# Kernel optimization log

Hardware: AMD Instinct MI355X
Metric: run time of the kernel (lower is better)

Reference implementation:

```python
import jax, jax.numpy as jnp
import numpy as np
from jax import lax


def _layernorm(x, scale, bias, eps=1e-5):
    m = x.mean(-1, keepdims=True)
    v = x.var(-1, keepdims=True)
    return (x - m) / jnp.sqrt(v + eps) * scale + bias


def setup_inputs() -> dict:
    key = jax.random.key(0)
    d = 21                      # code distance
    S = d * d - 1               # 440 tokens
    g = d + 1                   # 22x22 grid
    D, H, F, L, B = 256, 8, 512, 6, 64
    ks = jax.random.split(key, 24)
    w = 0.02
    idx = np.arange(S)
    scatter_positions = jnp.asarray(np.stack([idx // g, idx % g], axis=1), dtype=jnp.int64)
    inp = {
        'x': jax.random.randint(ks[0], (B, S), 0, 2).astype(jnp.int64),
        'scatter_positions': scatter_positions,
        'event_emb': w * jax.random.normal(ks[1], (2, D), jnp.float32),
        'pos_x': w * jax.random.normal(ks[2], (2 * d + 1, D), jnp.float32),
        'pos_y': w * jax.random.normal(ks[3], (2 * d + 1, D), jnp.float32),
        'stab_emb': w * jax.random.normal(ks[4], (2, D), jnp.float32),
        'tok_x': jax.random.randint(ks[5], (S,), 0, 2 * d + 1).astype(jnp.int64),
        'tok_y': jax.random.randint(ks[6], (S,), 0, 2 * d + 1).astype(jnp.int64),
        'tok_stab': jax.random.randint(ks[7], (S,), 0, 2).astype(jnp.int64),
        'attn_bias': w * jax.random.normal(ks[8], (S, S), jnp.float32),
        'Wqkv': w * jax.random.normal(ks[9], (L, 3 * D, D), jnp.float32),
        'bqkv': jnp.zeros((L, 3 * D), jnp.float32),
        'Wo': w * jax.random.normal(ks[10], (L, D, D), jnp.float32),
        'bo': jnp.zeros((L, D), jnp.float32),
        'W1': w * jax.random.normal(ks[11], (L, F, D), jnp.float32),
        'b1': jnp.zeros((L, F), jnp.float32),
        'W2': w * jax.random.normal(ks[12], (L, D, F), jnp.float32),
        'b2': jnp.zeros((L, D), jnp.float32),
        'ln1_s': jnp.ones((L, D), jnp.float32),
        'ln1_b': jnp.zeros((L, D), jnp.float32),
        'ln2_s': jnp.ones((L, D), jnp.float32),
        'ln2_b': jnp.zeros((L, D), jnp.float32),
        'cw1': w * jax.random.normal(ks[13], (L, D, D // H, 3, 3), jnp.float32),
        'cb1': jnp.zeros((L, D), jnp.float32),
        'cw2': w * jax.random.normal(ks[14], (L, D, D // H, 3, 3), jnp.float32),
        'cb2': jnp.zeros((L, D), jnp.float32),
        'cw3': w * jax.random.normal(ks[15], (L, D, D // H, 3, 3), jnp.float32),
        'cb3': jnp.zeros((L, D), jnp.float32),
    }
    return inp


def _forward(x, scatter_positions, event_emb, pos_x, pos_y, stab_emb, tok_x, tok_y,
             tok_stab, attn_bias, Wqkv, bqkv, Wo, bo, W1, b1, W2, b2,
             ln1_s, ln1_b, ln2_s, ln2_b, cw1, cb1, cw2, cb2, cw3, cb3):
    B, S = x.shape
    D = event_emb.shape[1]
    L = Wqkv.shape[0]
    H = D // cw1.shape[2]           # groups = n_heads
    dh = D // H
    g = int(np.sqrt(S + 1)) + 1     # (d+1) grid side
    rows = scatter_positions[:, 0]
    cols = scatter_positions[:, 1]

    # 2D positional encoding gathers + event embedding
    pos = pos_x[tok_x] + pos_y[tok_y] + stab_emb[tok_stab]   # [S, D]
    h = event_emb[x] + pos[None]                             # [B, S, D]

    scale = 1.0 / np.sqrt(dh).astype(np.float32)

    def conv(xg, wgt, b, dil):
        y = lax.conv_general_dilated(
            xg, wgt, window_strides=(1, 1), padding=[(dil, dil), (dil, dil)],
            rhs_dilation=(dil, dil), feature_group_count=H,
            dimension_numbers=('NCHW', 'OIHW', 'NCHW'))
        return jax.nn.relu(y + b[None, :, None, None])

    for l in range(L):
        # --- bias-MHA: QK^T * scale + learned relative bias, softmax, V ---
        qkv = jnp.einsum('bsd,ed->bse', h, Wqkv[l]) + bqkv[l]
        q, k, v = jnp.split(qkv, 3, axis=-1)
        q = q.reshape(B, S, H, dh)
        k = k.reshape(B, S, H, dh)
        v = v.reshape(B, S, H, dh)
        scores = jnp.einsum('bqhd,bkhd->bhqk', q, k) * scale + attn_bias[None, None]
        p = jax.nn.softmax(scores, axis=-1)
        o = jnp.einsum('bhqk,bkhd->bqhd', p, v).reshape(B, S, D)
        a = jnp.einsum('bsd,ed->bse', o, Wo[l]) + bo[l]
        h = _layernorm(h + a, ln1_s[l], ln1_b[l])
        # --- FFN (post-norm, ReLU) ---
        ff = jax.nn.relu(jnp.einsum('bsd,fd->bsf', h, W1[l]) + b1[l])
        ff = jnp.einsum('bsf,df->bsd', ff, W2[l]) + b2[l]
        h = _layernorm(h + ff, ln2_s[l], ln2_b[l])
        # --- scatter to 2D grid, grouped dilated convs, collect back ---
        grid = jnp.zeros((B, g, g, D), h.dtype).at[:, rows, cols].set(h)
        xg = grid.transpose(0, 3, 1, 2)                       # NCHW
        xg = 0.5 * (xg + conv(xg, cw1[l], cb1[l], 1)
                       + conv(xg, cw2[l], cb2[l], 2)
                       + conv(xg, cw3[l], cb3[l], 3))
        h = xg.transpose(0, 2, 3, 1)[:, rows, cols]           # collect_from_2d
    return h


def reference(x, scatter_positions, event_emb, pos_x, pos_y, stab_emb, tok_x, tok_y,
              tok_stab, attn_bias, Wqkv, bqkv, Wo, bo, W1, b1, W2, b2,
              ln1_s, ln1_b, ln2_s, ln2_b, cw1, cb1, cw2, cb2, cw3, cb3):
    return _forward(x, scatter_positions, event_emb, pos_x, pos_y, stab_emb, tok_x,
                    tok_y, tok_stab, attn_bias, Wqkv, bqkv, Wo, bo, W1, b1, W2, b2,
                    ln1_s, ln1_b, ln2_s, ln2_b, cw1, cb1, cw2, cb2, cw3, cb3)
```

## Files before the change

### kernel.cpp

```cpp
#include <hip/hip_runtime.h>
#include <hip/hip_bf16.h>

#define NB 64
#define S 440
#define D 256
#define H 8
#define DH 32
#define F 512
#define NL 6
#define G 22
#define NT (NB*S)
#define QBLK 224
#define QT2 2
#define PADK 456
#define CSTR 40

typedef __hip_bfloat16 bf16;
typedef unsigned short u16;
typedef __bf16 bf16x8 __attribute__((ext_vector_type(8)));
typedef float f32x4 __attribute__((ext_vector_type(4)));

#define MAGIC_BF16 0x3F803F80u

__device__ __align__(16) u16 g_abT[(S / 4) * S * 4];
#define WOFF_QKV 0
#define WOFF_WO  (NL*3*D*D)
#define WOFF_W1  (WOFF_WO + NL*D*D)
#define WOFF_W2  (WOFF_W1 + NL*F*D)
__device__ __align__(16) u16 g_wlin[WOFF_W2 + NL*D*F];
#define CVSTRIDE ((size_t)NL * 9 * 8 * 1024)
__device__ __align__(16) u16 g_cwt[3 * CVSTRIDE];
__device__ __align__(16) u16 g_qkvb[(size_t)NT * 768];
__device__ __align__(16) u16 g_obuf[(size_t)NT * D];
__device__ __align__(16) u16 g_acb [(size_t)NT * D];
__device__ __align__(16) u16 g_hbb [(size_t)NT * D];

static __device__ __forceinline__ float bf2f(bf16 x) { return __bfloat162float(x); }
static __device__ __forceinline__ float u2f(u16 u) {
  union { unsigned int i; float f; } t; t.i = ((unsigned int)u) << 16; return t.f;
}
static __device__ __forceinline__ float i2f(unsigned v) {
  union { unsigned u; float f; } t; t.u = v; return t.f;
}
static __device__ __forceinline__ u16 f2u(float f) {
  bf16 h = __float2bfloat16(f);
  return *(u16*)&h;
}
static __device__ __forceinline__ unsigned cvt_pk(float lo, float hi) {
  unsigned r;
  asm("v_cvt_pk_bf16_f32 %0, %1, %2" : "=v"(r) : "v"(lo), "v"(hi));
  return r;
}
static __device__ __forceinline__ float ldT(const void* p, size_t i, bool bfm) {
  return bfm ? u2f(((const u16*)p)[i]) : ((const float*)p)[i];
}
static __device__ __forceinline__ bf16x8 as_bf16x8(uint4 v) {
  union { uint4 u; bf16x8 b; } t; t.u = v; return t.b;
}
static __device__ __forceinline__ void gload_lds16(const u16* g, u16* l) {
  __builtin_amdgcn_global_load_lds(
      (const __attribute__((address_space(1))) void*)g,
      (__attribute__((address_space(3))) void*)l, 16, 0, 0);
}
static __device__ __forceinline__ const u16* selbuf(const void* ext, int sel) {
  return sel == 0 ? (const u16*)ext : sel == 1 ? g_hbb : sel == 2 ? g_qkvb : g_obuf;
}

__global__ void __launch_bounds__(256) cvt_conv(
    const void* __restrict__ src, int which, const unsigned* __restrict__ probe)
{
  bool bfm = (*probe == MAGIC_BF16);
  int n = NL * D * DH * 9;
  int i = blockIdx.x * 256 + threadIdx.x;
  if (i >= n) return;
  int kk = i % 9;
  int ic = (i / 9) % DH;
  int oc = (i / 288) % D;
  int l  = i / 73728;
  int g = oc >> 5, oc32 = oc & 31;
  u16 v;
  if (bfm) v = ((const u16*)src)[i];
  else     v = f2u(((const float*)src)[i]);
  g_cwt[(size_t)which * CVSTRIDE + (((size_t)l * 9 + kk) * 8 + g) * 1024 + oc32 * 32 + ic] = v;
}

__global__ void __launch_bounds__(256) cvt_lin(
    const void* __restrict__ src, size_t dstoff, int n,
    const unsigned* __restrict__ probe)
{
  bool bfm = (*probe == MAGIC_BF16);
  int i = blockIdx.x * 256 + threadIdx.x;
  if (i >= n) return;
  g_wlin[dstoff + i] = bfm ? ((const u16*)src)[i] : f2u(((const float*)src)[i]);
}

__global__ void __launch_bounds__(256) cvt_bias(
    const void* __restrict__ ab, const unsigned* __restrict__ probe)
{
  bool bfm = (*probe == MAGIC_BF16);
  int i = blockIdx.x * 256 + threadIdx.x;
  if (i >= (S / 4) * S * 4) return;
  int j = i & 3;
  int t = i >> 2;
  int q = t % S;
  int k4 = t / S;
  int k = k4 * 4 + j;
  float v = ldT(ab, (size_t)q * S + k, bfm) * 1.4426950408889634f;
  g_abT[i] = f2u(v);
}

__global__ void __launch_bounds__(256) embed_kernel(
    const int* __restrict__ x, const void* __restrict__ event_emb,
    const void* __restrict__ pos_x, const void* __restrict__ pos_y,
    const void* __restrict__ stab_emb, const int* __restrict__ tok_x,
    const int* __restrict__ tok_y, const int* __restrict__ tok_stab,
    bf16* __restrict__ h, const unsigned* __restrict__ probe)
{
  bool bfm = (*probe == MAGIC_BF16);
  int d = threadIdx.x;
#pragma unroll
  for (int r = 0; r < 4; ++r) {
    int t = blockIdx.x * 4 + r;
    int b = t / S, s = t - b * S;
    float v = ldT(event_emb, (size_t)x[b * S + s] * D + d, bfm)
            + ldT(pos_x, (size_t)tok_x[s] * D + d, bfm)
            + ldT(pos_y, (size_t)tok_y[s] * D + d, bfm)
            + ldT(stab_emb, (size_t)tok_stab[s] * D + d, bfm);
    h[(size_t)t * D + d] = __float2bfloat16(v);
  }
}

template <int RELU>
__global__ void __launch_bounds__(256) gemm_mfma(
    const void* __restrict__ Aext, int asel, size_t woff,
    const void* __restrict__ bias, size_t boff, int csel,
    int M, int N, int K, const unsigned* __restrict__ probe)
{
  bool bfm = (*probe == MAGIC_BF16);
  __shared__ u16 As[2][128][32];
  __shared__ u16 Ws[2][128][32];
  int tid = threadIdx.x;
  int bn = blockIdx.x, bm = blockIdx.y;
  int lane = tid & 63, w = tid >> 6;
  int wm = (w >> 1) * 64, wn = (w & 1) * 64;
  int qd = lane >> 4, ln16 = lane & 15;
  f32x4 zero4 = {0.f, 0.f, 0.f, 0.f};
  f32x4 acc[4][4];
#pragma unroll
  for (int i = 0; i < 4; ++i)
#pragma unroll
    for (int j = 0; j < 4; ++j) acc[i][j] = zero4;

  const u16* Au = selbuf(Aext, asel);
  u16* Cu = (csel == 0) ? g_qkvb : g_acb;
  const u16* Wu = g_wlin + woff;
  int srow = w * 32 + (lane >> 2);
  int skc  = (lane & 3) << 3;
  size_t abase = (size_t)(bm * 128 + srow) * K + skc;
  size_t wbase = (size_t)(bn * 128 + srow) * K + skc;

  gload_lds16(Au + abase,                   &As[0][w * 32][0]);
  gload_lds16(Au + abase + (size_t)16 * K,  &As[0][w * 32 + 16][0]);
  gload_lds16(Wu + wbase,                   &Ws[0][w * 32][0]);
  gload_lds16(Wu + wbase + (size_t)16 * K,  &Ws[0][w * 32 + 16][0]);

  int cur = 0;
  for (int k0 = 0; k0 < K; k0 += 32) {
    __syncthreads();
    if (k0 + 32 < K) {
      int nb = cur ^ 1;
      gload_lds16(Au + abase + k0 + 32,                  &As[nb][w * 32][0]);
      gload_lds16(Au + abase + (size_t)16 * K + k0 + 32, &As[nb][w * 32 + 16][0]);
      gload_lds16(Wu + wbase + k0 + 32,                  &Ws[nb][w * 32][0]);
      gload_lds16(Wu + wbase + (size_t)16 * K + k0 + 32, &Ws[nb][w * 32 + 16][0]);
    }
    bf16x8 af[4], bfr[4];
#pragma unroll
    for (int t = 0; t < 4; ++t) {
      af[t]  = *(const bf16x8*)&As[cur][wm + t * 16 + ln16][qd * 8];
      bfr[t] = *(const bf16x8*)&Ws[cur][wn + t * 16 + ln16][qd * 8];
    }
#pragma unroll
    for (int mt = 0; mt < 4; ++mt)
#pragma unroll
      for (int nt = 0; nt < 4; ++nt)
        acc[mt][nt] = __builtin_amdgcn_mfma_f32_16x16x32_bf16(af[mt], bfr[nt], acc[mt][nt], 0, 0, 0);
    cur ^= 1;
  }
#pragma unroll
  for (int nt = 0; nt < 4; ++nt) {
    int gcol = bn * 128 + wn + nt * 16 + ln16;
    float bv = ldT(bias, boff + gcol, bfm);
#pragma unroll
    for (int mt = 0; mt < 4; ++mt) {
#pragma unroll
      for (int r = 0; r < 4; ++r) {
        int grow = bm * 128 + wm + mt * 16 + qd * 4 + r;
        float v = acc[mt][nt][r] + bv;
        if (RELU) v = fmaxf(v, 0.f);
        Cu[(size_t)grow * N + gcol] = f2u(v);
      }
    }
  }
}

__global__ void __launch_bounds__(512) gemm_ln(
    const void* __restrict__ Aext, int asel, size_t woff,
    const void* __restrict__ bias, size_t boff,
    void* __restrict__ hext, int hsel,
    const void* __restrict__ sc, size_t soff,
    const void* __restrict__ bi, size_t boff2,
    int K, const unsigned* __restrict__ probe)
{
  bool bfm = (*probe == MAGIC_BF16);
  __shared__ u16 As[2][128][32];
  __shared__ u16 Ws[2][256][32];
  __shared__ float redS[4][128];
  __shared__ float redQ[4][128];
  int tid = threadIdx.x;
  int bm = blockIdx.x;
  int lane = tid & 63, w = tid >> 6;
  int wm = (w >> 2) * 64, wn = (w & 3) * 64;
  int qd = lane >> 4, ln16 = lane & 15;
  f32x4 zero4 = {0.f, 0.f, 0.f, 0.f};
  f32x4 acc[4][4];
#pragma unroll
  for (int i = 0; i < 4; ++i)
#pragma unroll
    for (int j = 0; j < 4; ++j) acc[i][j] = zero4;

  const u16* Au = selbuf(Aext, asel);
  u16* hp = hsel ? g_hbb : (u16*)hext;
  const u16* Wu = g_wlin + woff;
  int arow = w * 16 + (lane >> 2);
  int wrow = w * 32 + (lane >> 2);
  int skc  = (lane & 3) << 3;
  size_t abase = (size_t)(bm * 128 + arow) * K + skc;
  size_t wbase = (size_t)wrow * K + skc;

  gload_lds16(Au + abase,                  &As[0][w * 16][0]);
  gload_lds16(Wu + wbase,                  &Ws[0][w * 32][0]);
  gload_lds16(Wu + wbase + (size_t)16 * K, &Ws[0][w * 32 + 16][0]);

  int cur = 0;
  for (int k0 = 0; k0 < K; k0 += 32) {
    __syncthreads();
    if (k0 + 32 < K) {
      int nb = cur ^ 1;
      gload_lds16(Au + abase + k0 + 32,                  &As[nb][w * 16][0]);
      gload_lds16(Wu + wbase + k0 + 32,                  &Ws[nb][w * 32][0]);
      gload_lds16(Wu + wbase + (size_t)16 * K + k0 + 32, &Ws[nb][w * 32 + 16][0]);
    }
    bf16x8 af[4], bfr[4];
#pragma unroll
    for (int t = 0; t < 4; ++t) {
      af[t]  = *(const bf16x8*)&As[cur][wm + t * 16 + ln16][qd * 8];
      bfr[t] = *(const bf16x8*)&Ws[cur][wn + t * 16 + ln16][qd * 8];
    }
#pragma unroll
    for (int mt = 0; mt < 4; ++mt)
#pragma unroll
      for (int nt = 0; nt < 4; ++nt)
        acc[mt][nt] = __builtin_amdgcn_mfma_f32_16x16x32_bf16(af[mt], bfr[nt], acc[mt][nt], 0, 0, 0);
    cur ^= 1;
  }

  float bv[4];
#pragma unroll
  for (int nt = 0; nt < 4; ++nt) bv[nt] = ldT(bias, boff + wn + nt * 16 + ln16, bfm);
#pragma unroll
  for (int mt = 0; mt < 4; ++mt)
#pragma unroll
    for (int r = 0; r < 4; ++r) {
      size_t grow = (size_t)bm * 128 + wm + mt * 16 + qd * 4 + r;
#pragma unroll
      for (int nt = 0; nt < 4; ++nt) {
        int col = wn + nt * 16 + ln16;
        acc[mt][nt][r] += bv[nt] + u2f(hp[grow * D + col]);
      }
    }
#pragma unroll
  for (int mt = 0; mt < 4; ++mt)
#pragma unroll
    for (int r = 0; r < 4; ++r) {
      float s = (acc[mt][0][r] + acc[mt][1][r]) + (acc[mt][2][r] + acc[mt][3][r]);
      float q = (acc[mt][0][r] * acc[mt][0][r] + acc[mt][1][r] * acc[mt][1][r])
              + (acc[mt][2][r] * acc[mt][2][r] + acc[mt][3][r] * acc[mt][3][r]);
#pragma unroll
      for (int m = 1; m <= 8; m <<= 1) {
        s += __shfl_xor(s, m, 64);
        q += __shfl_xor(q, m, 64);
      }
      if (ln16 == 0) {
        int lrow = wm + mt * 16 + qd * 4 + r;
        redS[w & 3][lrow] = s;
        redQ[w & 3][lrow] = q;
      }
    }
  __syncthreads();
  float ls[4], lb[4];
#pragma unroll
  for (int nt = 0; nt < 4; ++nt) {
    ls[nt] = ldT(sc, soff + wn + nt * 16 + ln16, bfm);
    lb[nt] = ldT(bi, boff2 + wn + nt * 16 + ln16, bfm);
  }
#pragma unroll
  for (int mt = 0; mt < 4; ++mt)
#pragma unroll
    for (int r = 0; r < 4; ++r) {
      int lrow = wm + mt * 16 + qd * 4 + r;
      float Ssum = (redS[0][lrow] + redS[1][lrow]) + (redS[2][lrow] + redS[3][lrow]);
      float Qsum = (redQ[0][lrow] + redQ[1][lrow]) + (redQ[2][lrow] + redQ[3][lrow]);
      float mean = Ssum * (1.0f / D);
      float rstd = rsqrtf(Qsum * (1.0f / D) - mean * mean + 1e-5f);
      size_t grow = (size_t)bm * 128 + lrow;
#pragma unroll
      for (int nt = 0; nt < 4; ++nt) {
        int col = wn + nt * 16 + ln16;
        float o = (acc[mt][nt][r] - mean) * rstd * ls[nt] + lb[nt];
        hp[grow * D + col] = f2u(o);
      }
    }
}

__global__ void __launch_bounds__(448) attn_mfma()
{
  __shared__ u16 VT[32 * PADK];
  int tid = threadIdx.x;
  int blk = blockIdx.x;
  int qt = (blk >> 3) & 1;
  int bh = ((blk >> 4) << 3) | (blk & 7);
  int hh = bh % H;
  int b  = bh / H;
  int lane = tid & 63, w = tid >> 6;
  int qd = lane >> 4, ln16 = lane & 15;
  const u16* qkvu = g_qkvb;

  unsigned* VT32 = (unsigned*)VT;
#pragma unroll
  for (int i = 0; i < 2; ++i) {
    int slot = tid + i * 448;
    int rp = slot >> 2, kc = slot & 3;
    int r0 = rp * 2;
    uint4 va = make_uint4(0, 0, 0, 0), vb = make_uint4(0, 0, 0, 0);
    if (r0 < S)     va = *(const uint4*)&qkvu[((size_t)(b * S + r0)) * 768 + 512 + hh * DH + kc * 8];
    if (r0 + 1 < S) vb = *(const uint4*)&qkvu[((size_t)(b * S + r0 + 1)) * 768 + 512 + hh * DH + kc * 8];
    unsigned aw[4] = {va.x, va.y, va.z, va.w};
    unsigned bw[4] = {vb.x, vb.y, vb.z, vb.w};
#pragma unroll
    for (int jj = 0; jj < 4; ++jj) {
      int d = kc * 8 + jj * 2;
      VT32[(size_t)(d    ) * (PADK / 2) + rp] = (aw[jj] & 0xffffu) | ((bw[jj] & 0xffffu) << 16);
      VT32[(size_t)(d + 1) * (PADK / 2) + rp] = (aw[jj] >> 16)     | ((bw[jj] >> 16) << 16);
    }
  }

  int q0 = qt * QBLK + w * 32;
  int qaA = q0 + ln16;      if (qaA >= S) qaA = S - 1;
  int qaB = q0 + 16 + ln16; if (qaB >= S) qaB = S - 1;
  bf16x8 afA = *(const bf16x8*)&qkvu[((size_t)(b * S + qaA)) * 768 + hh * DH + qd * 8];
  bf16x8 afB = *(const bf16x8*)&qkvu[((size_t)(b * S + qaB)) * 768 + hh * DH + qd * 8];
  __syncthreads();

  int kperm = ((ln16 >> 2) << 3) + (ln16 & 3);
  auto kload = [&](int ks_, int half) -> uint4 {
    int tok = ks_ * 32 + kperm + half * 4;
    if (tok >= S) tok = S - 1;
    return *(const uint4*)&qkvu[((size_t)(b * S + tok)) * 768 + 256 + hh * DH + qd * 8];
  };
  uint4 kn0 = kload(0, 0), kn1 = kload(0, 1);

  float lsA = 0.f, lsB = 0.f;
  f32x4 zero4 = {0.f, 0.f, 0.f, 0.f};
  f32x4 oa0A = zero4, oa1A = zero4;
  f32x4 oa0B = zero4, oa1B = zero4;
  const float SC2 = 0.17677669529663689f * 1.4426950408889634f;

  auto bias4 = [&](uint2 wv, float* o) {
    o[0] = i2f(wv.x << 16); o[1] = i2f(wv.x & 0xffff0000u);
    o[2] = i2f(wv.y << 16); o[3] = i2f(wv.y & 0xffff0000u);
  };

  auto body = [&](int ks, bool masked) {
    int k4a = ks * 8 + 2 * qd;
    int k4b = k4a + 1;
    if (masked) { if (k4a > 109) k4a = 109; if (k4b > 109) k4b = 109; }
    uint2 bwaA = *(const uint2*)&g_abT[((size_t)k4a * S + qaA) * 4];
    uint2 bwbA = *(const uint2*)&g_abT[((size_t)k4b * S + qaA) * 4];
    uint2 bwaB = *(const uint2*)&g_abT[((size_t)k4a * S + qaB) * 4];
    uint2 bwbB = *(const uint2*)&g_abT[((size_t)k4b * S + qaB) * 4];
    bf16x8 kf0 = as_bf16x8(kn0), kf1 = as_bf16x8(kn1);
    if (!masked) { kn0 = kload(ks + 1, 0); kn1 = kload(ks + 1, 1); }
    __builtin_amdgcn_s_setprio(1);
    f32x4 s0A = __builtin_amdgcn_mfma_f32_16x16x32_bf16(kf0, afA, zero4, 0, 0, 0);
    f32x4 s1A = __builtin_amdgcn_mfma_f32_16x16x32_bf16(kf1, afA, zero4, 0, 0, 0);
    f32x4 s0B = __builtin_amdgcn_mfma_f32_16x16x32_bf16(kf0, afB, zero4, 0, 0, 0);
    f32x4 s1B = __builtin_amdgcn_mfma_f32_16x16x32_bf16(kf1, afB, zero4, 0, 0, 0);
    __builtin_amdgcn_s_setprio(0);
    float bAA[4], bBA[4], bAB[4], bBB[4];
    bias4(bwaA, bAA); bias4(bwbA, bBA); bias4(bwaB, bAB); bias4(bwbB, bBB);
    float pA[8], pB[8];
    if (!masked) {
#pragma unroll
      for (int r = 0; r < 4; ++r) {
        pA[r]     = exp2f(fminf(fmaf(s0A[r], SC2, bAA[r]), 80.f));
        pA[4 + r] = exp2f(fminf(fmaf(s1A[r], SC2, bBA[r]), 80.f));
        pB[r]     = exp2f(fminf(fmaf(s0B[r], SC2, bAB[r]), 80.f));
        pB[4 + r] = exp2f(fminf(fmaf(s1B[r], SC2, bBB[r]), 80.f));
      }
    } else {
      int c0 = ks * 32 + qd * 8;
#pragma unroll
      for (int r = 0; r < 4; ++r) {
        bool m0 = (c0 + r < S), m1 = (c0 + 4 + r < S);
        pA[r]     = exp2f(m0 ? fminf(fmaf(s0A[r], SC2, bAA[r]), 80.f) : -1e30f);
        pA[4 + r] = exp2f(m1 ? fminf(fmaf(s1A[r], SC2, bBA[r]), 80.f) : -1e30f);
        pB[r]     = exp2f(m0 ? fminf(fmaf(s0B[r], SC2, bAB[r]), 80.f) : -1e30f);
        pB[4 + r] = exp2f(m1 ? fminf(fmaf(s1B[r], SC2, bBB[r]), 80.f) : -1e30f);
      }
    }
    lsA += ((pA[0] + pA[1]) + (pA[2] + pA[3])) + ((pA[4] + pA[5]) + (pA[6] + pA[7]));
    lsB += ((pB[0] + pB[1]) + (pB[2] + pB[3])) + ((pB[4] + pB[5]) + (pB[6] + pB[7]));
    bf16x8 pfA = as_bf16x8(make_uint4(
        cvt_pk(pA[0], pA[1]), cvt_pk(pA[2], pA[3]),
        cvt_pk(pA[4], pA[5]), cvt_pk(pA[6], pA[7])));
    bf16x8 pfB = as_bf16x8(make_uint4(
        cvt_pk(pB[0], pB[1]), cvt_pk(pB[2], pB[3]),
        cvt_pk(pB[4], pB[5]), cvt_pk(pB[6], pB[7])));
    int kb = ks * 32;
    bf16x8 vf0 = *(const bf16x8*)&VT[(size_t)ln16 * PADK + kb + qd * 8];
    bf16x8 vf1 = *(const bf16x8*)&VT[(size_t)(16 + ln16) * PADK + kb + qd * 8];
    __builtin_amdgcn_s_setprio(1);
    oa0A = __builtin_amdgcn_mfma_f32_16x16x32_bf16(vf0, pfA, oa0A, 0, 0, 0);
    oa1A = __builtin_amdgcn_mfma_f32_16x16x32_bf16(vf1, pfA, oa1A, 0, 0, 0);
    oa0B = __builtin_amdgcn_mfma_f32_16x16x32_bf16(vf0, pfB, oa0B, 0, 0, 0);
    oa1B = __builtin_amdgcn_mfma_f32_16x16x32_bf16(vf1, pfB, oa1B, 0, 0, 0);
    __builtin_amdgcn_s_setprio(0);
  };

  for (int ks = 0; ks < 13; ++ks) body(ks, false);
  body(13, true);

  lsA += __shfl_xor(lsA, 16, 64);
  lsA += __shfl_xor(lsA, 32, 64);
  lsB += __shfl_xor(lsB, 16, 64);
  lsB += __shfl_xor(lsB, 32, 64);
  float invA = 1.0f / lsA, invB = 1.0f / lsB;
  int qA = q0 + ln16, qB = q0 + 16 + ln16;
  if (qA < S) {
    u16* op = g_obuf + ((size_t)(b * S + qA)) * D + hh * DH;
    *(uint2*)&op[qd * 4] = make_uint2(
        cvt_pk(oa0A[0] * invA, oa0A[1] * invA),
        cvt_pk(oa0A[2] * invA, oa0A[3] * invA));
    *(uint2*)&op[16 + qd * 4] = make_uint2(
        cvt_pk(oa1A[0] * invA, oa1A[1] * invA),
        cvt_pk(oa1A[2] * invA, oa1A[3] * invA));
  }
  if (qB < S) {
    u16* op = g_obuf + ((size_t)(b * S + qB)) * D + hh * DH;
    *(uint2*)&op[qd * 4] = make_uint2(
        cvt_pk(oa0B[0] * invB, oa0B[1] * invB),
        cvt_pk(oa0B[2] * invB, oa0B[3] * invB));
    *(uint2*)&op[16 + qd * 4] = make_uint2(
        cvt_pk(oa1B[0] * invB, oa1B[1] * invB),
        cvt_pk(oa1B[2] * invB, oa1B[3] * invB));
  }
}

__global__ void __launch_bounds__(256) conv_mfma(
    const void* __restrict__ hin_ext, int hinsel,
    const void* __restrict__ cb1, const void* __restrict__ cb2,
    const void* __restrict__ cb3, size_t cboff,
    void* __restrict__ hout_ext, int houtsel, int l, int final_,
    const unsigned* __restrict__ probe)
{
  bool bfm = (*probe == MAGIC_BF16);
  __shared__ u16 X[17 * 28 * CSTR];
  int half = blockIdx.x, g = blockIdx.y, b = blockIdx.z;
  int tid = threadIdx.x;
  int rb = half ? 7 : -3;
  const u16* hin = selbuf(hin_ext, hinsel);

  for (int i = tid; i < 17 * 28 * CSTR / 8; i += 256)
    *(uint4*)&X[i * 8] = make_uint4(0, 0, 0, 0);
  __syncthreads();
  int rv0 = half ? 7 : 0;
  int nrow = half ? 13 : 14;
  for (int i = tid; i < nrow * 22 * 4; i += 256) {
    int tk = i >> 2, ch = i & 3;
    int r = rv0 + tk / 22, c = tk % 22;
    uint4 v = *(const uint4*)&hin[((size_t)(b * S + r * 22 + c)) * D + g * 32 + ch * 8];
    *(uint4*)&X[(((r - rb) * 28) + (c + 3)) * CSTR + ch * 8] = v;
  }
  __syncthreads();

  int lane = tid & 63, w = tid >> 6;
  int qd = lane >> 4, ln16 = lane & 15;
  int nt = w & 1;
  int mq = w >> 1;
  int t_base = half * 224 + mq * 112;
  int oc_l = nt * 16 + ln16;

  int aoff[7];
#pragma unroll
  for (int mt = 0; mt < 7; ++mt) {
    int t = t_base + mt * 16 + ln16;
    if (t > S - 1) t = S - 1;
    int r = t / 22, c = t - r * 22;
    aoff[mt] = (((r - rb) * 28) + (c + 3)) * CSTR;
  }
  f32x4 fin[7];
#pragma unroll
  for (int mt = 0; mt < 7; ++mt) {
#pragma unroll
    for (int r4 = 0; r4 < 4; ++r4) {
      int t = t_base + mt * 16 + qd * 4 + r4;
      if (t > S - 1) t = S - 1;
      int r = t / 22, c = t - r * 22;
      fin[mt][r4] = u2f(X[(((r - rb) * 28) + (c + 3)) * CSTR + oc_l]);
    }
  }

  f32x4 zero4 = {0.f, 0.f, 0.f, 0.f};
  const void* cbs[3] = {cb1, cb2, cb3};
#pragma unroll
  for (int cv = 0; cv < 3; ++cv) {
    int dil = cv + 1;
    f32x4 acc[7];
#pragma unroll
    for (int mt = 0; mt < 7; ++mt) acc[mt] = zero4;
    const u16* wt = g_cwt + ((size_t)cv * NL + l) * (9 * 8 * 1024);
#pragma unroll
    for (int kk = 0; kk < 9; ++kk) {
      int off = ((kk / 3 - 1) * 28 + (kk % 3 - 1)) * dil * CSTR;
      bf16x8 bfrag = *(const bf16x8*)&wt[((size_t)kk * 8 + g) * 1024 + oc_l * 32 + qd * 8];
#pragma unroll
      for (int mt = 0; mt < 7; ++mt) {
        bf16x8 a = *(const bf16x8*)&X[aoff[mt] + off + qd * 8];
        acc[mt] = __builtin_amdgcn_mfma_f32_16x16x32_bf16(a, bfrag, acc[mt], 0, 0, 0);
      }
    }
    float bv = ldT(cbs[cv], cboff + g * 32 + oc_l, bfm);
#pragma unroll
    for (int mt = 0; mt < 7; ++mt)
#pragma unroll
      for (int r4 = 0; r4 < 4; ++r4)
        fin[mt][r4] += fmaxf(acc[mt][r4] + bv, 0.f);
  }

#pragma unroll
  for (int mt = 0; mt < 7; ++mt)
#pragma unroll
    for (int r4 = 0; r4 < 4; ++r4) {
      int t = t_base + mt * 16 + qd * 4 + r4;
      if (t < S) {
        float outv = 0.5f * fin[mt][r4];
        size_t oi = ((size_t)(b * S + t)) * D + g * 32 + oc_l;
        if (final_ && !bfm) ((float*)hout_ext)[oi] = outv;
        else {
          u16* ho = houtsel ? g_hbb : (u16*)hout_ext;
          ho[oi] = f2u(outv);
        }
      }
    }
}

extern "C" void kernel_launch(void* const* d_in, const int* in_sizes, int n_in,
                              void* d_out, int out_size, void* d_ws, size_t ws_size,
                              hipStream_t stream)
{
  const int*  x         = (const int*)d_in[0];
  const void* event_emb = d_in[2];
  const void* pos_x     = d_in[3];
  const void* pos_y     = d_in[4];
  const void* stab_emb  = d_in[5];
  const int*  tok_x     = (const int*)d_in[6];
  const int*  tok_y     = (const int*)d_in[7];
  const int*  tok_stab  = (const int*)d_in[8];
  const void* attn_bias = d_in[9];
  const void* Wqkv      = d_in[10];
  const void* bqkv      = d_in[11];
  const void* Wo        = d_in[12];
  const void* bo        = d_in[13];
  const void* W1        = d_in[14];
  const void* b1        = d_in[15];
  const void* W2        = d_in[16];
  const void* b2        = d_in[17];
  const void* ln1_s     = d_in[18];
  const void* ln1_b     = d_in[19];
  const void* ln2_s     = d_in[20];
  const void* ln2_b     = d_in[21];
  const void* cw1       = d_in[22];
  const void* cb1       = d_in[23];
  const void* cw2       = d_in[24];
  const void* cb2       = d_in[25];
  const void* cw3       = d_in[26];
  const void* cb3       = d_in[27];
  (void)in_sizes; (void)n_in; (void)out_size; (void)d_ws; (void)ws_size;
  const unsigned* probe = (const unsigned*)ln1_s;

  int ncv = NL * D * DH * 9;
  cvt_conv<<<(ncv + 255)/256, 256, 0, stream>>>(cw1, 0, probe);
  cvt_conv<<<(ncv + 255)/256, 256, 0, stream>>>(cw2, 1, probe);
  cvt_conv<<<(ncv + 255)/256, 256, 0, stream>>>(cw3, 2, probe);
  cvt_bias<<<((S/4)*S*4 + 255)/256, 256, 0, stream>>>(attn_bias, probe);
  cvt_lin<<<(NL*3*D*D + 255)/256, 256, 0, stream>>>(Wqkv, WOFF_QKV, NL*3*D*D, probe);
  cvt_lin<<<(NL*D*D   + 255)/256, 256, 0, stream>>>(Wo,   WOFF_WO,  NL*D*D,   probe);
  cvt_lin<<<(NL*F*D   + 255)/256, 256, 0, stream>>>(W1,   WOFF_W1,  NL*F*D,   probe);
  cvt_lin<<<(NL*D*F   + 255)/256, 256, 0, stream>>>(W2,   WOFF_W2,  NL*D*F,   probe);

  bf16* hout_ = (bf16*)d_out;
  embed_kernel<<<NT/4, 256, 0, stream>>>(x, event_emb, pos_x, pos_y, stab_emb,
                                         tok_x, tok_y, tok_stab, hout_, probe);

  for (int l = 0; l < NL; ++l) {
    int hs = l & 1;
    int fin = (l == NL - 1) ? 1 : 0;
    gemm_mfma<0><<<dim3(6, NT/128), 256, 0, stream>>>(
        hout_, hs, (size_t)WOFF_QKV + (size_t)l*3*D*D, bqkv, (size_t)l*3*D, 0,
        NT, 3*D, D, probe);
    attn_mfma<<<NB*H*QT2, 448, 0, stream>>>();
    gemm_ln<<<NT/128, 512, 0, stream>>>(
        hout_, 3, (size_t)WOFF_WO + (size_t)l*D*D, bo, (size_t)l*D,
        hout_, hs, ln1_s, (size_t)l*D, ln1_b, (size_t)l*D, D, probe);
    gemm_mfma<1><<<dim3(4, NT/128), 256, 0, stream>>>(
        hout_, hs, (size_t)WOFF_W1 + (size_t)l*F*D, b1, (size_t)l*F, 0,
        NT, F, D, probe);
    gemm_ln<<<NT/128, 512, 0, stream>>>(
        hout_, 2, (size_t)WOFF_W2 + (size_t)l*D*F, b2, (size_t)l*D,
        hout_, hs, ln2_s, (size_t)l*D, ln2_b, (size_t)l*D, F, probe);
    conv_mfma<<<dim3(2, 8, NB), 256, 0, stream>>>(
        hout_, hs, cb1, cb2, cb3, (size_t)l*D, hout_, hs ^ 1, l, fin, probe);
  }
}
```

Before: 1.241 ms.

## Swizzle GEMM block order, shrink LN-GEMM tile to 64 rows, raise conv MFMA priority

The plain GEMM now runs on a 1D grid whose block index is remapped so that groups of 8 row-tiles are visited together per column tile, padded to 224 row groups with early exit. The aim is better L2 reuse of A and W tiles. The fused GEMM+LayerNorm kernel moves from 128-row tiles with 512 threads to 64-row tiles with 256 threads, doubling the block count to fill more CUs, at the cost of reloading the full weight tile twice as often. The conv kernel wraps its MFMA loop in s_setprio to favour matrix issue over other waves.

Measured after the change: 1.339 ms. +7.9%, slower.

```diff
diff --git a/kernel.cpp b/kernel.cpp
--- a/kernel.cpp
+++ b/kernel.cpp
@@ -14,6 +14,8 @@
 #define QT2 2
 #define PADK 456
 #define CSTR 40
+#define MT128 (NT/128)
+#define MT128P 224
 
 typedef __hip_bfloat16 bf16;
 typedef unsigned short u16;
@@ -139,8 +141,13 @@
   bool bfm = (*probe == MAGIC_BF16);
   __shared__ u16 As[2][128][32];
   __shared__ u16 Ws[2][128][32];
+  int nbn = N >> 7;
+  int id = blockIdx.x;
+  int r8 = id & 7, kq = id >> 3;
+  int bm = (kq / nbn) * 8 + r8;
+  int bn = kq % nbn;
+  if (bm >= (M >> 7)) return;
   int tid = threadIdx.x;
-  int bn = blockIdx.x, bm = blockIdx.y;
   int lane = tid & 63, w = tid >> 6;
   int wm = (w >> 1) * 64, wn = (w & 1) * 64;
   int qd = lane >> 4, ln16 = lane & 15;
@@ -204,7 +211,7 @@
   }
 }
 
-__global__ void __launch_bounds__(512) gemm_ln(
+__global__ void __launch_bounds__(256) gemm_ln(
     const void* __restrict__ Aext, int asel, size_t woff,
     const void* __restrict__ bias, size_t boff,
     void* __restrict__ hext, int hsel,
@@ -213,14 +220,14 @@
     int K, const unsigned* __restrict__ probe)
 {
   bool bfm = (*probe == MAGIC_BF16);
-  __shared__ u16 As[2][128][32];
+  __shared__ u16 As[2][64][32];
   __shared__ u16 Ws[2][256][32];
-  __shared__ float redS[4][128];
-  __shared__ float redQ[4][128];
+  __shared__ float redS[4][64];
+  __shared__ float redQ[4][64];
   int tid = threadIdx.x;
   int bm = blockIdx.x;
   int lane = tid & 63, w = tid >> 6;
-  int wm = (w >> 2) * 64, wn = (w & 3) * 64;
+  int wn = w * 64;
   int qd = lane >> 4, ln16 = lane & 15;
   f32x4 zero4 = {0.f, 0.f, 0.f, 0.f};
   f32x4 acc[4][4];
@@ -233,14 +240,16 @@
   u16* hp = hsel ? g_hbb : (u16*)hext;
   const u16* Wu = g_wlin + woff;
   int arow = w * 16 + (lane >> 2);
-  int wrow = w * 32 + (lane >> 2);
+  int wrow = w * 64 + (lane >> 2);
   int skc  = (lane & 3) << 3;
-  size_t abase = (size_t)(bm * 128 + arow) * K + skc;
+  size_t abase = (size_t)(bm * 64 + arow) * K + skc;
   size_t wbase = (size_t)wrow * K + skc;
 
   gload_lds16(Au + abase,                  &As[0][w * 16][0]);
-  gload_lds16(Wu + wbase,                  &Ws[0][w * 32][0]);
-  gload_lds16(Wu + wbase + (size_t)16 * K, &Ws[0][w * 32 + 16][0]);
+  gload_lds16(Wu + wbase,                  &Ws[0][w * 64][0]);
+  gload_lds16(Wu + wbase + (size_t)16 * K, &Ws[0][w * 64 + 16][0]);
+  gload_lds16(Wu + wbase + (size_t)32 * K, &Ws[0][w * 64 + 32][0]);
+  gload_lds16(Wu + wbase + (size_t)48 * K, &Ws[0][w * 64 + 48][0]);
 
   int cur = 0;
   for (int k0 = 0; k0 < K; k0 += 32) {
@@ -248,13 +257,15 @@
     if (k0 + 32 < K) {
       int nb = cur ^ 1;
       gload_lds16(Au + abase + k0 + 32,                  &As[nb][w * 16][0]);
-      gload_lds16(Wu + wbase + k0 + 32,                  &Ws[nb][w * 32][0]);
-      gload_lds16(Wu + wbase + (size_t)16 * K + k0 + 32, &Ws[nb][w * 32 + 16][0]);
+      gload_lds16(Wu + wbase + k0 + 32,                  &Ws[nb][w * 64][0]);
+      gload_lds16(Wu + wbase + (size_t)16 * K + k0 + 32, &Ws[nb][w * 64 + 16][0]);
+      gload_lds16(Wu + wbase + (size_t)32 * K + k0 + 32, &Ws[nb][w * 64 + 32][0]);
+      gload_lds16(Wu + wbase + (size_t)48 * K + k0 + 32, &Ws[nb][w * 64 + 48][0]);
     }
     bf16x8 af[4], bfr[4];
 #pragma unroll
     for (int t = 0; t < 4; ++t) {
-      af[t]  = *(const bf16x8*)&As[cur][wm + t * 16 + ln16][qd * 8];
+      af[t]  = *(const bf16x8*)&As[cur][t * 16 + ln16][qd * 8];
       bfr[t] = *(const bf16x8*)&Ws[cur][wn + t * 16 + ln16][qd * 8];
     }
 #pragma unroll
@@ -272,7 +283,7 @@
   for (int mt = 0; mt < 4; ++mt)
 #pragma unroll
     for (int r = 0; r < 4; ++r) {
-      size_t grow = (size_t)bm * 128 + wm + mt * 16 + qd * 4 + r;
+      size_t grow = (size_t)bm * 64 + mt * 16 + qd * 4 + r;
 #pragma unroll
       for (int nt = 0; nt < 4; ++nt) {
         int col = wn + nt * 16 + ln16;
@@ -292,9 +303,9 @@
         q += __shfl_xor(q, m, 64);
       }
       if (ln16 == 0) {
-        int lrow = wm + mt * 16 + qd * 4 + r;
-        redS[w & 3][lrow] = s;
-        redQ[w & 3][lrow] = q;
+        int lrow = mt * 16 + qd * 4 + r;
+        redS[w][lrow] = s;
+        redQ[w][lrow] = q;
       }
     }
   __syncthreads();
@@ -308,12 +319,12 @@
   for (int mt = 0; mt < 4; ++mt)
 #pragma unroll
     for (int r = 0; r < 4; ++r) {
-      int lrow = wm + mt * 16 + qd * 4 + r;
+      int lrow = mt * 16 + qd * 4 + r;
       float Ssum = (redS[0][lrow] + redS[1][lrow]) + (redS[2][lrow] + redS[3][lrow]);
       float Qsum = (redQ[0][lrow] + redQ[1][lrow]) + (redQ[2][lrow] + redQ[3][lrow]);
       float mean = Ssum * (1.0f / D);
       float rstd = rsqrtf(Qsum * (1.0f / D) - mean * mean + 1e-5f);
-      size_t grow = (size_t)bm * 128 + lrow;
+      size_t grow = (size_t)bm * 64 + lrow;
 #pragma unroll
       for (int nt = 0; nt < 4; ++nt) {
         int col = wn + nt * 16 + ln16;
@@ -534,11 +545,13 @@
     for (int kk = 0; kk < 9; ++kk) {
       int off = ((kk / 3 - 1) * 28 + (kk % 3 - 1)) * dil * CSTR;
       bf16x8 bfrag = *(const bf16x8*)&wt[((size_t)kk * 8 + g) * 1024 + oc_l * 32 + qd * 8];
+      __builtin_amdgcn_s_setprio(1);
 #pragma unroll
       for (int mt = 0; mt < 7; ++mt) {
         bf16x8 a = *(const bf16x8*)&X[aoff[mt] + off + qd * 8];
         acc[mt] = __builtin_amdgcn_mfma_f32_16x16x32_bf16(a, bfrag, acc[mt], 0, 0, 0);
       }
+      __builtin_amdgcn_s_setprio(0);
     }
     float bv = ldT(cbs[cv], cboff + g * 32 + oc_l, bfm);
 #pragma unroll
@@ -616,17 +629,17 @@
   for (int l = 0; l < NL; ++l) {
     int hs = l & 1;
     int fin = (l == NL - 1) ? 1 : 0;
-    gemm_mfma<0><<<dim3(6, NT/128), 256, 0, stream>>>(
+    gemm_mfma<0><<<MT128P * 6, 256, 0, stream>>>(
         hout_, hs, (size_t)WOFF_QKV + (size_t)l*3*D*D, bqkv, (size_t)l*3*D, 0,
         NT, 3*D, D, probe);
     attn_mfma<<<NB*H*QT2, 448, 0, stream>>>();
-    gemm_ln<<<NT/128, 512, 0, stream>>>(
+    gemm_ln<<<NT/64, 256, 0, stream>>>(
         hout_, 3, (size_t)WOFF_WO + (size_t)l*D*D, bo, (size_t)l*D,
         hout_, hs, ln1_s, (size_t)l*D, ln1_b, (size_t)l*D, D, probe);
-    gemm_mfma<1><<<dim3(4, NT/128), 256, 0, stream>>>(
+    gemm_mfma<1><<<MT128P * 4, 256, 0, stream>>>(
         hout_, hs, (size_t)WOFF_W1 + (size_t)l*F*D, b1, (size_t)l*F, 0,
         NT, F, D, probe);
-    gemm_ln<<<NT/128, 512, 0, stream>>>(
+    gemm_ln<<<NT/64, 256, 0, stream>>>(
         hout_, 2, (size_t)WOFF_W2 + (size_t)l*D*F, b2, (size_t)l*D,
         hout_, hs, ln2_s, (size_t)l*D, ln2_b, (size_t)l*D, F, probe);
     conv_mfma<<<dim3(2, 8, NB), 256, 0, stream>>>(
```
